# Kernel tuning notes

Measured on AMD Instinct MI355X. Metric: run time of the kernel, lower is better.

The kernel has to match this reference:

```python
import jax, jax.numpy as jnp
import numpy as np

B, T, C, H = 4, 2048, 1024, 16
D = C // H  # head dim = 64


def setup_inputs() -> dict:
    key = jax.random.key(0)
    ks = jax.random.split(key, 8)
    s = 1.0 / np.sqrt(C)
    return {
        "x": jax.random.normal(ks[0], (B, T, C), jnp.float32),
        "mask": jax.random.randint(ks[1], (B, T), 0, 2, jnp.int32),
        "Wq": jax.random.normal(ks[2], (C, C), jnp.float32) * s,
        "bq": jnp.zeros((C,), jnp.float32),
        "Wk": jax.random.normal(ks[3], (C, C), jnp.float32) * s,
        "bk": jnp.zeros((C,), jnp.float32),
        "Wv": jax.random.normal(ks[4], (C, C), jnp.float32) * s,
        "bv": jnp.zeros((C,), jnp.float32),
    }


def reference(x, mask, Wq, bq, Wk, bk, Wv, bv):
    # QKV projections (nn.Linear: x @ W.T + b); W stored here as [out,in] -> use W.T
    q = x @ Wq.T + bq
    k = x @ Wk.T + bk
    v = x @ Wv.T + bv
    # split heads: [B,T,C] -> [B,H,T,D]
    q = q.reshape(B, T, H, D).transpose(0, 2, 1, 3)
    k = k.reshape(B, T, H, D).transpose(0, 2, 1, 3)
    v = v.reshape(B, T, H, D).transpose(0, 2, 1, 3)
    # scaled dot-product attention scores [B,H,T,T]
    attn = jnp.einsum("bhqd,bhkd->bhqk", q, k) / jnp.sqrt(jnp.float32(D))
    # additive mask over key positions: attn - inf*(1-mask), expressed stably
    big_neg = jnp.float32(-1e30)
    attn = jnp.where(mask[:, None, None, :] > 0, attn, big_neg)
    attn = jax.nn.softmax(attn, axis=-1)
    # dropout p=0 -> identity
    y = jnp.einsum("bhqk,bhkd->bhqd", attn, v)
    # merge heads: [B,H,T,D] -> [B,T,C]
    return y.transpose(0, 2, 1, 3).reshape(B, T, C)
```

## Files before the change

kernel.cpp:

```cpp
#include <hip/hip_runtime.h>
#include <stdint.h>

#define BB 4
#define TT 2048
#define CC 1024
#define HH 16
#define DD 64
#define MM (BB * TT)

typedef unsigned short u16;
typedef unsigned int   u32;
typedef __attribute__((ext_vector_type(8))) short short8;
typedef _Float16 half8  __attribute__((ext_vector_type(8)));
typedef __fp16   fp16x2 __attribute__((ext_vector_type(2)));
typedef __attribute__((ext_vector_type(4))) float f32x4;
typedef __attribute__((ext_vector_type(4))) unsigned short u16x4;
typedef __attribute__((ext_vector_type(4))) unsigned int u32x4;

#if __has_builtin(__builtin_amdgcn_exp2f)
#define EXP2(x) __builtin_amdgcn_exp2f(x)
#else
#define EXP2(x) __expf(0.69314718055994531f * (x))
#endif

__device__ inline u16 f2bf(float f) {
    union { float f; unsigned u; } v; v.f = f;
    unsigned r = 0x7fffu + ((v.u >> 16) & 1u);
    return (u16)((v.u + r) >> 16);
}
__device__ inline u16 f2h(float f) {
    union { _Float16 h; u16 u; } c; c.h = (_Float16)f; return c.u;
}
__device__ inline u32 pkh(float a, float b) {
    union { fp16x2 h; u32 u; } c;
    c.h = __builtin_amdgcn_cvt_pkrtz(a, b);
    return c.u;
}

#define NX (MM * CC / 4)
#define NW (CC * CC / 4)
__global__ void cvt_all(const float* __restrict__ x,  const float* __restrict__ Wq,
                        const float* __restrict__ Wk, const float* __restrict__ Wv,
                        u16* __restrict__ xb, u16* __restrict__ Wb) {
    int i = blockIdx.x * blockDim.x + threadIdx.x;
    const float* src; u16* dst; int j;
    if (i < NX)               { src = x;  dst = xb;                       j = i; }
    else if (i < NX + NW)     { src = Wq; dst = Wb;                       j = i - NX; }
    else if (i < NX + 2 * NW) { src = Wk; dst = Wb + (size_t)CC * CC;     j = i - NX - NW; }
    else if (i < NX + 3 * NW) { src = Wv; dst = Wb + (size_t)2 * CC * CC; j = i - NX - 2 * NW; }
    else return;
    float4 v = ((const float4*)src)[j];
    u16x4 o;
    o.x = f2bf(v.x); o.y = f2bf(v.y); o.z = f2bf(v.z); o.w = f2bf(v.w);
    ((u16x4*)dst)[j] = o;
}

__global__ void qkv_gemm(const u16* __restrict__ xb, const u16* __restrict__ Wb,
                         const float* __restrict__ bq, const float* __restrict__ bk,
                         const float* __restrict__ bv,
                         u16* __restrict__ Qh, u16* __restrict__ Kh, u16* __restrict__ Vt)
{
    const int z = blockIdx.z;
    const u16* W = Wb + (size_t)z * CC * CC;
    const float* bias = (z == 0) ? bq : ((z == 1) ? bk : bv);
    const float scale = (z == 0) ? 0.18033688011112042f : 1.0f;

    __shared__ __align__(16) u16 As[128][32];
    __shared__ __align__(16) u16 Bs[128][32];

    const int tid = threadIdx.x;
    const int l  = tid & 63, w = tid >> 6;
    const int wm = w >> 1,  wn = w & 1;
    const int lr = l & 15,  lq = l >> 4;
    const int m0 = blockIdx.y * 128, n0 = blockIdx.x * 128;

    f32x4 acc[4][4] = {};

    const u16* aLDS = (z == 2) ? &As[0][0] : &Bs[0][0];
    const u16* bLDS = (z == 2) ? &Bs[0][0] : &As[0][0];

    for (int kt = 0; kt < CC; kt += 32) {
        __syncthreads();
        #pragma unroll
        for (int r = 0; r < 2; ++r) {
            int c   = (r * 4 + w) * 64 + l;
            int row = c >> 2, kc = c & 3;
            const u16* ga = xb + (size_t)(m0 + row) * CC + kt + kc * 8;
            __builtin_amdgcn_global_load_lds(
                (const __attribute__((address_space(1))) void*)ga,
                (__attribute__((address_space(3))) void*)(&As[0][0] + (size_t)c * 8), 16, 0, 0);
            const u16* gb = W + (size_t)(n0 + row) * CC + kt + kc * 8;
            __builtin_amdgcn_global_load_lds(
                (const __attribute__((address_space(1))) void*)gb,
                (__attribute__((address_space(3))) void*)(&Bs[0][0] + (size_t)c * 8), 16, 0, 0);
        }
        __syncthreads();

        short8 af[4], bfr[4];
        #pragma unroll
        for (int mi = 0; mi < 4; ++mi)
            af[mi] = *(const short8*)(aLDS + (size_t)(wm * 64 + mi * 16 + lr) * 32 + lq * 8);
        #pragma unroll
        for (int ni = 0; ni < 4; ++ni)
            bfr[ni] = *(const short8*)(bLDS + (size_t)(wn * 64 + ni * 16 + lr) * 32 + lq * 8);
        #pragma unroll
        for (int mi = 0; mi < 4; ++mi)
            #pragma unroll
            for (int ni = 0; ni < 4; ++ni)
                acc[mi][ni] = __builtin_amdgcn_mfma_f32_16x16x32_bf16(
                    af[mi], bfr[ni], acc[mi][ni], 0, 0, 0);
    }

    if (z == 2) {
        #pragma unroll
        for (int ni = 0; ni < 4; ++ni) {
            int n = n0 + wn * 64 + ni * 16 + lr;
            float bvv = bias[n];
            int h = n >> 6, d = n & 63;
            #pragma unroll
            for (int mi = 0; mi < 4; ++mi) {
                int mbase = m0 + wm * 64 + mi * 16 + lq * 4;
                int b = mbase >> 11, t0 = mbase & (TT - 1);
                u16x4 pkv;
                #pragma unroll
                for (int r = 0; r < 4; ++r)
                    pkv[r] = f2h(acc[mi][ni][r] + bvv);
                *(u16x4*)&Vt[((size_t)(b * HH + h) * DD + d) * TT + t0] = pkv;
            }
        }
    } else {
        u16* out = (z == 0) ? Qh : Kh;
        #pragma unroll
        for (int mi = 0; mi < 4; ++mi) {
            int nb = n0 + wm * 64 + mi * 16 + lq * 4;
            float4 b4 = *(const float4*)&bias[nb];
            int h = nb >> 6, d0 = nb & 63;
            #pragma unroll
            for (int ni = 0; ni < 4; ++ni) {
                int m = m0 + wn * 64 + ni * 16 + lr;
                int b = m >> 11, t = m & (TT - 1);
                u16x4 pkv;
                pkv.x = f2h((acc[mi][ni][0] + b4.x) * scale);
                pkv.y = f2h((acc[mi][ni][1] + b4.y) * scale);
                pkv.z = f2h((acc[mi][ni][2] + b4.z) * scale);
                pkv.w = f2h((acc[mi][ni][3] + b4.w) * scale);
                *(u16x4*)&out[((size_t)(b * HH + h) * TT + t) * DD + d0] = pkv;
            }
        }
    }
}

__global__ __launch_bounds__(256, 4)
void attn_kernel(const u16* __restrict__ Qh, const u16* __restrict__ Kh,
                 const u16* __restrict__ Vt, const int* __restrict__ mask,
                 float* __restrict__ out)
{
    const int qt = blockIdx.x;
    const int h  = blockIdx.y;
    const int b  = blockIdx.z;
    const int tid = threadIdx.x;
    const int l  = tid & 63, w = tid >> 6;
    const int lr = l & 15,  lq = l >> 4;

    __shared__ __align__(16) u16 Ks[2][32][72];
    __shared__ __align__(16) u16 Vs[2][80][40];

    const size_t base = (size_t)(b * HH + h) * TT * DD;
    const int q0 = qt * 128 + w * 32;

    half8 qf[2][2];
    #pragma unroll
    for (int qg = 0; qg < 2; ++qg)
        #pragma unroll
        for (int c = 0; c < 2; ++c)
            qf[qg][c] = *(const half8*)(Qh + base + (size_t)(q0 + qg * 16 + lr) * DD
                                        + c * 32 + lq * 8);

    const int kk = tid >> 3, dc = tid & 7;
    u16* k_dst0 = &Ks[0][kk][dc * 8];
    const u16* k_base = Kh + base + (size_t)kk * DD + dc * 8;
    const int vd = tid >> 2, vck = tid & 3;
    const int s0c = ((2 * vck) & 3) * 8 + (vck >> 1) * 4;
    const int s1c = ((2 * vck + 1) & 3) * 8 + (vck >> 1) * 4;
    u16* v_dst0a = &Vs[0][vd][s0c];
    u16* v_dst0b = &Vs[0][vd][s1c];
    const u16* v_base = Vt + base + (size_t)vd * TT + vck * 8;
    const int* mbase_p = mask + b * TT + 4 * lq;

    for (int i = tid; i < 16 * 40; i += 256) {
        (&Vs[0][64][0])[i] = 0x3C00;
        (&Vs[1][64][0])[i] = 0x3C00;
    }

    {
        half8 k0 = *(const half8*)k_base;
        half8 v0 = *(const half8*)v_base;
        *(half8*)k_dst0 = k0;
        u16x4 va = { (u16)((u32x4&)v0)[0], (u16)(((u32x4&)v0)[0] >> 16),
                     (u16)((u32x4&)v0)[1], (u16)(((u32x4&)v0)[1] >> 16) };
        u16x4 vb = { (u16)((u32x4&)v0)[2], (u16)(((u32x4&)v0)[2] >> 16),
                     (u16)((u32x4&)v0)[3], (u16)(((u32x4&)v0)[3] >> 16) };
        *(u16x4*)v_dst0a = va;
        *(u16x4*)v_dst0b = vb;
    }

    f32x4 o[2][5] = {};

    const int NT = TT / 32;
    __syncthreads();

    for (int kt = 0; kt < NT; ++kt) {
        const int p = kt & 1;
        int ktn = (kt + 1 < NT) ? kt + 1 : NT - 1;
        half8 kreg = *(const half8*)(k_base + (size_t)ktn * 32 * DD);
        half8 vreg = *(const half8*)(v_base + ktn * 32);
        int4 ma = *(const int4*)(mbase_p + kt * 32);
        int4 mb = *(const int4*)(mbase_p + kt * 32 + 16);

        half8 kf[2][2];
        #pragma unroll
        for (int kg = 0; kg < 2; ++kg)
            #pragma unroll
            for (int c = 0; c < 2; ++c)
                kf[kg][c] = *(const half8*)&Ks[p][kg * 16 + lr][c * 32 + lq * 8];

        f32x4 s[2][2];
        #pragma unroll
        for (int kg = 0; kg < 2; ++kg)
            #pragma unroll
            for (int qg = 0; qg < 2; ++qg) {
                f32x4 zz = {};
                zz = __builtin_amdgcn_mfma_f32_16x16x32_f16(kf[kg][0], qf[qg][0], zz, 0, 0, 0);
                zz = __builtin_amdgcn_mfma_f32_16x16x32_f16(kf[kg][1], qf[qg][1], zz, 0, 0, 0);
                s[kg][qg] = zz;
            }

        const u32 am0 = ((u32)(-ma.x) & 0xFFFFu) | ((u32)(-ma.y) << 16);
        const u32 am1 = ((u32)(-ma.z) & 0xFFFFu) | ((u32)(-ma.w) << 16);
        const u32 am2 = ((u32)(-mb.x) & 0xFFFFu) | ((u32)(-mb.y) << 16);
        const u32 am3 = ((u32)(-mb.z) & 0xFFFFu) | ((u32)(-mb.w) << 16);

        half8 pf[2];
        #pragma unroll
        for (int qg = 0; qg < 2; ++qg) {
            u32x4 pk;
            pk[0] = pkh(EXP2(s[0][qg][0]), EXP2(s[0][qg][1])) & am0;
            pk[1] = pkh(EXP2(s[0][qg][2]), EXP2(s[0][qg][3])) & am1;
            pk[2] = pkh(EXP2(s[1][qg][0]), EXP2(s[1][qg][1])) & am2;
            pk[3] = pkh(EXP2(s[1][qg][2]), EXP2(s[1][qg][3])) & am3;
            pf[qg] = (half8&)pk;
        }

        #pragma unroll
        for (int dg = 0; dg < 5; ++dg) {
            half8 vf = *(const half8*)&Vs[p][dg * 16 + lr][lq * 8];
            #pragma unroll
            for (int qg = 0; qg < 2; ++qg)
                o[qg][dg] = __builtin_amdgcn_mfma_f32_16x16x32_f16(pf[qg], vf, o[qg][dg], 0, 0, 0);
        }

        *(half8*)(k_dst0 + (p ^ 1) * (32 * 72)) = kreg;
        u16x4 va = { (u16)((u32x4&)vreg)[0], (u16)(((u32x4&)vreg)[0] >> 16),
                     (u16)((u32x4&)vreg)[1], (u16)(((u32x4&)vreg)[1] >> 16) };
        u16x4 vb = { (u16)((u32x4&)vreg)[2], (u16)(((u32x4&)vreg)[2] >> 16),
                     (u16)((u32x4&)vreg)[3], (u16)(((u32x4&)vreg)[3] >> 16) };
        *(u16x4*)(v_dst0a + (p ^ 1) * (80 * 40)) = va;
        *(u16x4*)(v_dst0b + (p ^ 1) * (80 * 40)) = vb;
        __syncthreads();
    }

    #pragma unroll
    for (int qg = 0; qg < 2; ++qg)
        #pragma unroll
        for (int r = 0; r < 4; ++r) {
            float inv = 1.f / o[qg][4][r];
            int t = q0 + qg * 16 + lq * 4 + r;
            float* op = out + (size_t)(b * TT + t) * CC + h * DD;
            #pragma unroll
            for (int dg = 0; dg < 4; ++dg)
                op[dg * 16 + lr] = o[qg][dg][r] * inv;
        }
}

extern "C" void kernel_launch(void* const* d_in, const int* in_sizes, int n_in,
                              void* d_out, int out_size, void* d_ws, size_t ws_size,
                              hipStream_t stream) {
    const float* x    = (const float*)d_in[0];
    const int*   mask = (const int*)d_in[1];
    const float* Wq   = (const float*)d_in[2];
    const float* bq   = (const float*)d_in[3];
    const float* Wk   = (const float*)d_in[4];
    const float* bk   = (const float*)d_in[5];
    const float* Wv   = (const float*)d_in[6];
    const float* bv   = (const float*)d_in[7];
    float* out = (float*)d_out;

    u16* xb = (u16*)d_ws;
    u16* Wb = xb + (size_t)MM * CC;
    u16* Qh = Wb + (size_t)3 * CC * CC;
    u16* Kh = Qh + (size_t)MM * CC;
    u16* Vt = Kh + (size_t)MM * CC;

    {
        int total = NX + 3 * NW;
        cvt_all<<<(total + 255) / 256, 256, 0, stream>>>(x, Wq, Wk, Wv, xb, Wb);
    }

    qkv_gemm<<<dim3(CC / 128, MM / 128, 3), 256, 0, stream>>>(xb, Wb, bq, bk, bv, Qh, Kh, Vt);

    attn_kernel<<<dim3(TT / 128, HH, BB), 256, 0, stream>>>(Qh, Kh, Vt, mask, out);
}
```

Baseline: 259.6 us.

## Double key tile to 64, use register ones for row sums, remap blocks per XCD

The attention kernel now processes 64 keys per iteration instead of 32, halving the number of loop iterations and __syncthreads barriers. The constant row of ones used to accumulate the softmax denominator moves from shared memory into a register operand. Block indices are remapped so that all query tiles of a given (batch, head) land on the same XCD, which should improve L2 reuse of K/V. The cost is a larger LDS footprint and higher register pressure, which may reduce occupancy.

New measurement: 257.7 us. No clear change (-0.7%).

```diff
diff --git a/kernel.cpp b/kernel.cpp
--- a/kernel.cpp
+++ b/kernel.cpp
@@ -35,6 +35,9 @@
     union { fp16x2 h; u32 u; } c;
     c.h = __builtin_amdgcn_cvt_pkrtz(a, b);
     return c.u;
+}
+__device__ inline u32 pkmask(int a, int b) {
+    return ((u32)(-a) & 0xFFFFu) | ((u32)(-b) << 16);
 }
 
 #define NX (MM * CC / 4)
@@ -155,15 +158,18 @@
                  const u16* __restrict__ Vt, const int* __restrict__ mask,
                  float* __restrict__ out)
 {
-    const int qt = blockIdx.x;
-    const int h  = blockIdx.y;
-    const int b  = blockIdx.z;
+    const int f   = blockIdx.x + (TT / 128) * (blockIdx.y + HH * blockIdx.z);
+    const int xcd = f & 7, g = f >> 3;
+    const int bh  = xcd * 8 + (g >> 4);
+    const int qt  = g & 15;
+    const int b   = bh >> 4, h = bh & 15;
+
     const int tid = threadIdx.x;
     const int l  = tid & 63, w = tid >> 6;
     const int lr = l & 15,  lq = l >> 4;
 
-    __shared__ __align__(16) u16 Ks[2][32][72];
-    __shared__ __align__(16) u16 Vs[2][80][40];
+    __shared__ __align__(16) u16 Ks[2][64][72];
+    __shared__ __align__(16) u16 Vs[2][2][64][40];
 
     const size_t base = (size_t)(b * HH + h) * TT * DD;
     const int q0 = qt * 128 + w * 32;
@@ -182,51 +188,68 @@
     const int vd = tid >> 2, vck = tid & 3;
     const int s0c = ((2 * vck) & 3) * 8 + (vck >> 1) * 4;
     const int s1c = ((2 * vck + 1) & 3) * 8 + (vck >> 1) * 4;
-    u16* v_dst0a = &Vs[0][vd][s0c];
-    u16* v_dst0b = &Vs[0][vd][s1c];
+    u16* v_dst0a = &Vs[0][0][vd][s0c];
+    u16* v_dst0b = &Vs[0][0][vd][s1c];
     const u16* v_base = Vt + base + (size_t)vd * TT + vck * 8;
     const int* mbase_p = mask + b * TT + 4 * lq;
 
-    for (int i = tid; i < 16 * 40; i += 256) {
-        (&Vs[0][64][0])[i] = 0x3C00;
-        (&Vs[1][64][0])[i] = 0x3C00;
-    }
+    const int VHALF = 64 * 40;
+    const int VBUF  = 2 * VHALF;
+    const int KHALF = 32 * 72;
+    const int KBUF  = 64 * 72;
+
+    union { u32 u[4]; half8 h; } one_u;
+    one_u.u[0] = one_u.u[1] = one_u.u[2] = one_u.u[3] = 0x3C003C00u;
+    const half8 ones = one_u.h;
 
     {
         half8 k0 = *(const half8*)k_base;
+        half8 k1 = *(const half8*)(k_base + 32 * DD);
         half8 v0 = *(const half8*)v_base;
+        half8 v1 = *(const half8*)(v_base + 32);
         *(half8*)k_dst0 = k0;
-        u16x4 va = { (u16)((u32x4&)v0)[0], (u16)(((u32x4&)v0)[0] >> 16),
-                     (u16)((u32x4&)v0)[1], (u16)(((u32x4&)v0)[1] >> 16) };
-        u16x4 vb = { (u16)((u32x4&)v0)[2], (u16)(((u32x4&)v0)[2] >> 16),
-                     (u16)((u32x4&)v0)[3], (u16)(((u32x4&)v0)[3] >> 16) };
-        *(u16x4*)v_dst0a = va;
-        *(u16x4*)v_dst0b = vb;
+        *(half8*)(k_dst0 + KHALF) = k1;
+        #pragma unroll
+        for (int hf = 0; hf < 2; ++hf) {
+            half8 vv = hf ? v1 : v0;
+            u16x4 va = { (u16)((u32x4&)vv)[0], (u16)(((u32x4&)vv)[0] >> 16),
+                         (u16)((u32x4&)vv)[1], (u16)(((u32x4&)vv)[1] >> 16) };
+            u16x4 vb = { (u16)((u32x4&)vv)[2], (u16)(((u32x4&)vv)[2] >> 16),
+                         (u16)((u32x4&)vv)[3], (u16)(((u32x4&)vv)[3] >> 16) };
+            *(u16x4*)(v_dst0a + hf * VHALF) = va;
+            *(u16x4*)(v_dst0b + hf * VHALF) = vb;
+        }
     }
 
     f32x4 o[2][5] = {};
 
-    const int NT = TT / 32;
+    const int NT = TT / 64;
     __syncthreads();
 
     for (int kt = 0; kt < NT; ++kt) {
         const int p = kt & 1;
         int ktn = (kt + 1 < NT) ? kt + 1 : NT - 1;
-        half8 kreg = *(const half8*)(k_base + (size_t)ktn * 32 * DD);
-        half8 vreg = *(const half8*)(v_base + ktn * 32);
-        int4 ma = *(const int4*)(mbase_p + kt * 32);
-        int4 mb = *(const int4*)(mbase_p + kt * 32 + 16);
-
-        half8 kf[2][2];
-        #pragma unroll
-        for (int kg = 0; kg < 2; ++kg)
+        const u16* kp = k_base + (size_t)ktn * 64 * DD;
+        half8 kreg0 = *(const half8*)kp;
+        half8 kreg1 = *(const half8*)(kp + 32 * DD);
+        const u16* vp = v_base + ktn * 64;
+        half8 vreg0 = *(const half8*)vp;
+        half8 vreg1 = *(const half8*)(vp + 32);
+        int4 m0 = *(const int4*)(mbase_p + kt * 64);
+        int4 m1 = *(const int4*)(mbase_p + kt * 64 + 16);
+        int4 m2 = *(const int4*)(mbase_p + kt * 64 + 32);
+        int4 m3 = *(const int4*)(mbase_p + kt * 64 + 48);
+
+        half8 kf[4][2];
+        #pragma unroll
+        for (int kg = 0; kg < 4; ++kg)
             #pragma unroll
             for (int c = 0; c < 2; ++c)
                 kf[kg][c] = *(const half8*)&Ks[p][kg * 16 + lr][c * 32 + lq * 8];
 
-        f32x4 s[2][2];
-        #pragma unroll
-        for (int kg = 0; kg < 2; ++kg)
+        f32x4 s[4][2];
+        #pragma unroll
+        for (int kg = 0; kg < 4; ++kg)
             #pragma unroll
             for (int qg = 0; qg < 2; ++qg) {
                 f32x4 zz = {};
@@ -235,37 +258,52 @@
                 s[kg][qg] = zz;
             }
 
-        const u32 am0 = ((u32)(-ma.x) & 0xFFFFu) | ((u32)(-ma.y) << 16);
-        const u32 am1 = ((u32)(-ma.z) & 0xFFFFu) | ((u32)(-ma.w) << 16);
-        const u32 am2 = ((u32)(-mb.x) & 0xFFFFu) | ((u32)(-mb.y) << 16);
-        const u32 am3 = ((u32)(-mb.z) & 0xFFFFu) | ((u32)(-mb.w) << 16);
-
-        half8 pf[2];
-        #pragma unroll
-        for (int qg = 0; qg < 2; ++qg) {
-            u32x4 pk;
-            pk[0] = pkh(EXP2(s[0][qg][0]), EXP2(s[0][qg][1])) & am0;
-            pk[1] = pkh(EXP2(s[0][qg][2]), EXP2(s[0][qg][3])) & am1;
-            pk[2] = pkh(EXP2(s[1][qg][0]), EXP2(s[1][qg][1])) & am2;
-            pk[3] = pkh(EXP2(s[1][qg][2]), EXP2(s[1][qg][3])) & am3;
-            pf[qg] = (half8&)pk;
-        }
-
-        #pragma unroll
-        for (int dg = 0; dg < 5; ++dg) {
-            half8 vf = *(const half8*)&Vs[p][dg * 16 + lr][lq * 8];
+        u32 am[8];
+        am[0] = pkmask(m0.x, m0.y); am[1] = pkmask(m0.z, m0.w);
+        am[2] = pkmask(m1.x, m1.y); am[3] = pkmask(m1.z, m1.w);
+        am[4] = pkmask(m2.x, m2.y); am[5] = pkmask(m2.z, m2.w);
+        am[6] = pkmask(m3.x, m3.y); am[7] = pkmask(m3.z, m3.w);
+
+        half8 pf[2][2];
+        #pragma unroll
+        for (int hf = 0; hf < 2; ++hf)
+            #pragma unroll
+            for (int qg = 0; qg < 2; ++qg) {
+                u32x4 pk;
+                pk[0] = pkh(EXP2(s[2*hf][qg][0]),   EXP2(s[2*hf][qg][1]))   & am[4*hf];
+                pk[1] = pkh(EXP2(s[2*hf][qg][2]),   EXP2(s[2*hf][qg][3]))   & am[4*hf+1];
+                pk[2] = pkh(EXP2(s[2*hf+1][qg][0]), EXP2(s[2*hf+1][qg][1])) & am[4*hf+2];
+                pk[3] = pkh(EXP2(s[2*hf+1][qg][2]), EXP2(s[2*hf+1][qg][3])) & am[4*hf+3];
+                pf[hf][qg] = (half8&)pk;
+            }
+
+        #pragma unroll
+        for (int hf = 0; hf < 2; ++hf) {
+            #pragma unroll
+            for (int dg = 0; dg < 4; ++dg) {
+                half8 vf = *(const half8*)&Vs[p][hf][dg * 16 + lr][lq * 8];
+                #pragma unroll
+                for (int qg = 0; qg < 2; ++qg)
+                    o[qg][dg] = __builtin_amdgcn_mfma_f32_16x16x32_f16(pf[hf][qg], vf, o[qg][dg], 0, 0, 0);
+            }
             #pragma unroll
             for (int qg = 0; qg < 2; ++qg)
-                o[qg][dg] = __builtin_amdgcn_mfma_f32_16x16x32_f16(pf[qg], vf, o[qg][dg], 0, 0, 0);
-        }
-
-        *(half8*)(k_dst0 + (p ^ 1) * (32 * 72)) = kreg;
-        u16x4 va = { (u16)((u32x4&)vreg)[0], (u16)(((u32x4&)vreg)[0] >> 16),
-                     (u16)((u32x4&)vreg)[1], (u16)(((u32x4&)vreg)[1] >> 16) };
-        u16x4 vb = { (u16)((u32x4&)vreg)[2], (u16)(((u32x4&)vreg)[2] >> 16),
-                     (u16)((u32x4&)vreg)[3], (u16)(((u32x4&)vreg)[3] >> 16) };
-        *(u16x4*)(v_dst0a + (p ^ 1) * (80 * 40)) = va;
-        *(u16x4*)(v_dst0b + (p ^ 1) * (80 * 40)) = vb;
+                o[qg][4] = __builtin_amdgcn_mfma_f32_16x16x32_f16(pf[hf][qg], ones, o[qg][4], 0, 0, 0);
+        }
+
+        u16* kd = k_dst0 + (p ^ 1) * KBUF;
+        *(half8*)kd = kreg0;
+        *(half8*)(kd + KHALF) = kreg1;
+        #pragma unroll
+        for (int hf = 0; hf < 2; ++hf) {
+            half8 vv = hf ? vreg1 : vreg0;
+            u16x4 va = { (u16)((u32x4&)vv)[0], (u16)(((u32x4&)vv)[0] >> 16),
+                         (u16)((u32x4&)vv)[1], (u16)(((u32x4&)vv)[1] >> 16) };
+            u16x4 vb = { (u16)((u32x4&)vv)[2], (u16)(((u32x4&)vv)[2] >> 16),
+                         (u16)((u32x4&)vv)[3], (u16)(((u32x4&)vv)[3] >> 16) };
+            *(u16x4*)(v_dst0a + (p ^ 1) * VBUF + hf * VHALF) = va;
+            *(u16x4*)(v_dst0b + (p ^ 1) * VBUF + hf * VHALF) = vb;
+        }
         __syncthreads();
     }
 
```
